# Optimization experiments

Hardware: AMD Instinct MI355X
Metric: run time of the kernel (lower is better)

## Reference

```python
import jax, jax.numpy as jnp
import numpy as np
from jax import lax

B, L, N_NODES, N_SEQ = 256, 15360, 16, 64


def _lstm_layer(x, wih, whh, bih, bhh):
    # x: (B, T, I); torch gate order i, f, g, o
    H = whh.shape[1]
    b = bih + bhh
    def step(carry, xt):
        h, c = carry
        gates = xt @ wih.T + h @ whh.T + b
        i, f, g, o = jnp.split(gates, 4, axis=-1)
        c = jax.nn.sigmoid(f) * c + jax.nn.sigmoid(i) * jnp.tanh(g)
        h = jax.nn.sigmoid(o) * jnp.tanh(c)
        return (h, c), h
    h0 = jnp.zeros((x.shape[0], H), x.dtype)
    _, ys = lax.scan(step, (h0, h0), x.transpose(1, 0, 2))
    return ys.transpose(1, 0, 2)


def setup_inputs() -> dict:
    ks = iter(jax.random.split(jax.random.key(0), 64))
    def rn(shape, scale=1.0):
        return (jax.random.normal(next(ks), shape) * scale).astype(jnp.float32)
    d = {"x": rn((B, 1, L))}
    chs = [1, 16, 32, 64]
    for i in range(3):
        cin, cout = chs[i], chs[i + 1]
        s = 1.0 / np.sqrt(cin * 5)
        d[f"cw{i}"] = rn((cout, cin, 5), s)
        d[f"cb{i}"] = rn((cout,), s)
        d[f"bng{i}"] = jnp.ones((cout,), jnp.float32)
        d[f"bnb{i}"] = jnp.zeros((cout,), jnp.float32)
        d[f"bnm{i}"] = jnp.zeros((cout,), jnp.float32)
        d[f"bnv{i}"] = jnp.ones((cout,), jnp.float32)
    Hh = 64
    for l in range(2):
        s = 1.0 / np.sqrt(Hh)
        d[f"wih{l}"] = rn((4 * Hh, 64), s)
        d[f"whh{l}"] = rn((4 * Hh, Hh), s)
        d[f"bih{l}"] = rn((4 * Hh,), s)
        d[f"bhh{l}"] = rn((4 * Hh,), s)
    gin = [256, 64, 64]
    for l in range(3):
        s = 1.0 / np.sqrt(gin[l])
        d[f"gw{l}"] = rn((64, gin[l]), s)
        d[f"gb{l}"] = rn((64,), s)
    d["clw"] = rn((5, 64), 0.125)
    d["clb"] = rn((5,), 0.125)
    return d


def reference(x, cw0, cb0, bng0, bnb0, bnm0, bnv0, cw1, cb1, bng1, bnb1, bnm1, bnv1, cw2, cb2, bng2, bnb2, bnm2, bnv2, wih0, whh0, bih0, bhh0, wih1, whh1, bih1, bhh1, gw0, gb0, gw1, gb1, gw2, gb2, clw, clb):
    h = x
    # CNN: [Conv1d(k=5,p=2) -> BN(eval) -> ReLU -> MaxPool(2)] x 3
    for cw, cb, g, b, m, v in ((cw0, cb0, bng0, bnb0, bnm0, bnv0),
                               (cw1, cb1, bng1, bnb1, bnm1, bnv1),
                               (cw2, cb2, bng2, bnb2, bnm2, bnv2)):
        h = lax.conv_general_dilated(h, cw, (1,), [(2, 2)], dimension_numbers=("NCH", "OIH", "NCH")) + cb[None, :, None]
        h = g[None, :, None] * (h - m[None, :, None]) * lax.rsqrt(v[None, :, None] + 1e-5) + b[None, :, None]
        h = jax.nn.relu(h)
        Bq, Cq, Lq = h.shape
        h = h.reshape(Bq, Cq, Lq // 2, 2).max(-1)
    # AdaptiveAvgPool1d(64): length divisible by 64 -> exact mean bins
    Bq, Cq, Lq = h.shape
    h = h.reshape(Bq, Cq, N_SEQ, Lq // N_SEQ).mean(-1)
    h = h.transpose(0, 2, 1)  # (B, 64, 64) = (batch, seq, channels)
    # 2-layer LSTM (dropout is identity in eval)
    h = _lstm_layer(h, wih0, whh0, bih0, bhh0)
    h = _lstm_layer(h, wih1, whh1, bih1, bhh1)
    # Graph builder: Pearson-style correlation + value thresholding
    Hf = h.reshape(Bq, -1)
    fpn = Hf.shape[1] // N_NODES  # 256 features per node
    nf = Hf[:, :N_NODES * fpn].reshape(Bq, N_NODES, fpn)
    cen = nf - nf.mean(-1, keepdims=True)
    nrm = cen / (jnp.std(cen, axis=-1, ddof=1, keepdims=True) + 1e-8)
    C = jnp.einsum("bnf,bmf->bnm", nrm, nrm) / fpn  # (B, N, N)
    Cf = C.reshape(Bq, -1)
    k = min(max(1, int((100.0 - 25.0) / 100.0 * Cf.shape[1])), Cf.shape[1] - 1)
    thr = jnp.sort(Cf, axis=1)[:, k - 1]  # torch.kthvalue(k)
    eye = jnp.eye(N_NODES, dtype=C.dtype)
    adj = (C > thr[:, None, None]).astype(C.dtype) * (1.0 - eye)
    # GCN: x = ReLU(W (x + A x) + b), 3 layers, then max over nodes
    g = nf
    for gw, gb in ((gw0, gb0), (gw1, gb1), (gw2, gb2)):
        g = jax.nn.relu((g + jnp.einsum("bnm,bmf->bnf", adj, g)) @ gw.T + gb)
    emb = g.max(axis=1)
    return emb @ clw.T + clb
```

## Files before the change

kernel.cpp:

```cpp
#include <hip/hip_runtime.h>
#include <math.h>

typedef __attribute__((ext_vector_type(2))) float v2f;

__global__ __launch_bounds__(256) void prep_weights_kernel(
    const float* __restrict__ cw0, const float* __restrict__ cb0,
    const float* __restrict__ bng0, const float* __restrict__ bnb0,
    const float* __restrict__ bnm0, const float* __restrict__ bnv0,
    const float* __restrict__ cw1, const float* __restrict__ cb1,
    const float* __restrict__ bng1, const float* __restrict__ bnb1,
    const float* __restrict__ bnm1, const float* __restrict__ bnv1,
    const float* __restrict__ cw2, const float* __restrict__ cb2,
    const float* __restrict__ bng2, const float* __restrict__ bnb2,
    const float* __restrict__ bnm2, const float* __restrict__ bnv2,
    float* __restrict__ wt1, float* __restrict__ b1,
    float* __restrict__ wt2, float* __restrict__ b2,
    float* __restrict__ w0f, float* __restrict__ b0f)
{
    int tid = threadIdx.x;
    for (int i = tid; i < 2560; i += 256) {
        int co = i & 31, r = i >> 5, t = r % 5, ci = r / 5;
        float s = bng1[co] * rsqrtf(bnv1[co] + 1e-5f);
        wt1[i] = cw1[(co * 16 + ci) * 5 + t] * s;
    }
    if (tid < 32) {
        float s = bng1[tid] * rsqrtf(bnv1[tid] + 1e-5f);
        b1[tid] = (cb1[tid] - bnm1[tid]) * s + bnb1[tid];
    }
    for (int i = tid; i < 10240; i += 256) {
        int co = i & 63, r = i >> 6, t = r % 5, ci = r / 5;
        float s = bng2[co] * rsqrtf(bnv2[co] + 1e-5f);
        wt2[i] = cw2[(co * 32 + ci) * 5 + t] * s;
    }
    if (tid < 64) {
        float s = bng2[tid] * rsqrtf(bnv2[tid] + 1e-5f);
        b2[tid] = (cb2[tid] - bnm2[tid]) * s + bnb2[tid];
    }
    if (tid < 80) {
        int co = tid / 5;
        float s = bng0[co] * rsqrtf(bnv0[co] + 1e-5f);
        w0f[tid] = cw0[tid] * s;
    }
    if (tid < 16) {
        float s = bng0[tid] * rsqrtf(bnv0[tid] + 1e-5f);
        b0f[tid] = (cb0[tid] - bnm0[tid]) * s + bnb0[tid];
    }
}

__global__ __launch_bounds__(256) void conv01_kernel(
    const float* __restrict__ x, const float* __restrict__ wt1,
    const float* __restrict__ b1, const float* __restrict__ w0f,
    const float* __restrict__ b0f, float* __restrict__ out)
{
    __shared__ float raw[528];
    __shared__ float xt0[16][260];
    __shared__ float w0l[80];
    __shared__ float b0l[16];
    int b = blockIdx.y, tid = threadIdx.x;
    int j0 = blockIdx.x * 128;
    const float* xb = x + (size_t)b * 15360;
    for (int p = tid; p < 524; p += 256) {
        int g = 4 * j0 - 6 + p;
        raw[p] = (g >= 0 && g < 15360) ? xb[g] : 0.f;
    }
    if (tid < 80) w0l[tid] = w0f[tid];
    if (tid < 16) b0l[tid] = b0f[tid];
    __syncthreads();
    {
        int ci0 = tid >> 4, sub = tid & 15;
        float w0 = w0l[ci0 * 5 + 0], w1 = w0l[ci0 * 5 + 1], w2 = w0l[ci0 * 5 + 2],
              w3 = w0l[ci0 * 5 + 3], w4 = w0l[ci0 * 5 + 4];
        float bb = b0l[ci0];
        for (int p = sub; p < 260; p += 16) {
            int q = 2 * j0 - 2 + p;
            float v = 0.f;
            if (q >= 0 && q < 7680) {
                float r0 = raw[2*p], r1 = raw[2*p+1], r2 = raw[2*p+2],
                      r3 = raw[2*p+3], r4 = raw[2*p+4], r5 = raw[2*p+5];
                float s0 = fmaf(w0, r0, fmaf(w1, r1, fmaf(w2, r2, fmaf(w3, r3, w4 * r4))));
                float s1 = fmaf(w0, r1, fmaf(w1, r2, fmaf(w2, r3, fmaf(w3, r4, w4 * r5))));
                v = fmaxf(fmaxf(s0, s1) + bb, 0.f);
            }
            xt0[ci0][p] = v;
        }
    }
    __syncthreads();
    int cg = tid >> 7, jj = tid & 127;
    int cgu = __builtin_amdgcn_readfirstlane(cg);
    const float* wb = wt1 + cgu * 16;
    v2f a0[8], a1[8];
#pragma unroll
    for (int q = 0; q < 8; ++q) { a0[q] = (v2f){0.f, 0.f}; a1[q] = (v2f){0.f, 0.f}; }
#pragma unroll 4
    for (int ci = 0; ci < 16; ++ci) {
        const float2* xr = reinterpret_cast<const float2*>(&xt0[ci][0]);
        float2 xA = xr[jj], xB = xr[jj + 1], xC = xr[jj + 2];
        float xv[6] = { xA.x, xA.y, xB.x, xB.y, xC.x, xC.y };
#pragma unroll
        for (int t = 0; t < 5; ++t) {
            const v2f* wp2 = reinterpret_cast<const v2f*>(wb + (ci * 5 + t) * 32);
            v2f va = { xv[t], xv[t] };
            v2f vc = { xv[t + 1], xv[t + 1] };
#pragma unroll
            for (int q2 = 0; q2 < 8; ++q2) {
                v2f w = wp2[q2];
                a0[q2] = __builtin_elementwise_fma(w, va, a0[q2]);
                a1[q2] = __builtin_elementwise_fma(w, vc, a1[q2]);
            }
        }
    }
    int j = j0 + jj;
    size_t obase = ((size_t)b * 32 + cgu * 16) * 3840 + j;
#pragma unroll
    for (int q2 = 0; q2 < 8; ++q2) {
#pragma unroll
        for (int cpp = 0; cpp < 2; ++cpp) {
            int q = 2 * q2 + cpp;
            float vb = b1[cgu * 16 + q];
            float m = fmaxf(a0[q2][cpp], a1[q2][cpp]) + vb;
            out[obase + (size_t)q * 3840] = fmaxf(m, 0.f);
        }
    }
}

__global__ __launch_bounds__(256) void conv2p_kernel(
    const float* __restrict__ in, const float* __restrict__ wt2,
    const float* __restrict__ b2, float* __restrict__ xs)
{
    __shared__ float xt[32 * 132];
    int b = blockIdx.y, tid = threadIdx.x;
    int j0 = blockIdx.x * 60;
    {
        int ci = tid >> 3, lane8 = tid & 7;
        const float* src = in + ((size_t)b * 32 + ci) * 3840;
        for (int p = lane8; p < 132; p += 8) {
            int gp = 2 * j0 - 2 + p;
            xt[ci * 132 + p] = (gp >= 0 && gp < 3840) ? src[gp] : 0.f;
        }
    }
    __syncthreads();
    int cg = tid >> 6, jj = tid & 63;
    int cgu = __builtin_amdgcn_readfirstlane(cg);
    const float* wb = wt2 + cgu * 16;
    v2f a0[8], a1[8];
#pragma unroll
    for (int q = 0; q < 8; ++q) { a0[q] = (v2f){0.f, 0.f}; a1[q] = (v2f){0.f, 0.f}; }
#pragma unroll 4
    for (int ci = 0; ci < 32; ++ci) {
        const float2* xr = reinterpret_cast<const float2*>(xt + ci * 132);
        float2 xA = xr[jj], xB = xr[jj + 1], xC = xr[jj + 2];
        float xv[6] = { xA.x, xA.y, xB.x, xB.y, xC.x, xC.y };
#pragma unroll
        for (int t = 0; t < 5; ++t) {
            const v2f* wp2 = reinterpret_cast<const v2f*>(wb + (ci * 5 + t) * 64);
            v2f va = { xv[t], xv[t] };
            v2f vc = { xv[t + 1], xv[t + 1] };
#pragma unroll
            for (int q2 = 0; q2 < 8; ++q2) {
                v2f w = wp2[q2];
                a0[q2] = __builtin_elementwise_fma(w, va, a0[q2]);
                a1[q2] = __builtin_elementwise_fma(w, vc, a1[q2]);
            }
        }
    }
    __syncthreads();
    float* outt = xt;
    if (jj < 60) {
#pragma unroll
        for (int q2 = 0; q2 < 8; ++q2) {
#pragma unroll
            for (int cpp = 0; cpp < 2; ++cpp) {
                int q = 2 * q2 + cpp;
                int co = cgu * 16 + q;
                float m = fmaxf(a0[q2][cpp], a1[q2][cpp]) + b2[co];
                outt[co * 61 + jj] = fmaxf(m, 0.f);
            }
        }
    }
    __syncthreads();
    if (tid < 128) {
        int co = tid & 63, bin = tid >> 6;
        const float* r = outt + co * 61 + bin * 30;
        float s = 0.f;
#pragma unroll
        for (int k = 0; k < 30; ++k) s += r[k];
        xs[((size_t)b * 64 + (blockIdx.x * 2 + bin)) * 64 + co] = s * (1.f / 30.f);
    }
}

__global__ __launch_bounds__(256) void lstm_kernel(
    const float* __restrict__ xseq,
    const float* __restrict__ wih0, const float* __restrict__ whh0,
    const float* __restrict__ bih0, const float* __restrict__ bhh0,
    const float* __restrict__ wih1, const float* __restrict__ whh1,
    const float* __restrict__ bih1, const float* __restrict__ bhh1,
    float* __restrict__ hseq)
{
    __shared__ float xb[64][64];
    __shared__ float xg[64][256];
    __shared__ float gb4[4][64];
    __shared__ float hb[64];
    int b = blockIdx.x;
    int tid = threadIdx.x;
    int wv = tid >> 6, ln = tid & 63;
    for (int i = tid; i < 4096; i += 256) xb[i >> 6][i & 63] = xseq[(size_t)b * 4096 + i];
    __syncthreads();
    float wr[64];
    for (int layer = 0; layer < 2; ++layer) {
        const float* wih = layer ? wih1 : wih0;
        const float* whh = layer ? whh1 : whh0;
        float bias = layer ? (bih1[tid] + bhh1[tid]) : (bih0[tid] + bhh0[tid]);
#pragma unroll
        for (int k4 = 0; k4 < 16; ++k4) {
            float4 v = reinterpret_cast<const float4*>(wih + (size_t)tid * 64)[k4];
            wr[k4 * 4 + 0] = v.x; wr[k4 * 4 + 1] = v.y;
            wr[k4 * 4 + 2] = v.z; wr[k4 * 4 + 3] = v.w;
        }
        for (int t = 0; t < 64; ++t) {
            float s0 = bias, s1 = 0.f, s2 = 0.f, s3 = 0.f;
#pragma unroll
            for (int k = 0; k < 64; k += 4) {
                s0 = fmaf(wr[k + 0], xb[t][k + 0], s0);
                s1 = fmaf(wr[k + 1], xb[t][k + 1], s1);
                s2 = fmaf(wr[k + 2], xb[t][k + 2], s2);
                s3 = fmaf(wr[k + 3], xb[t][k + 3], s3);
            }
            xg[t][tid] = (s0 + s1) + (s2 + s3);
        }
#pragma unroll
        for (int k4 = 0; k4 < 16; ++k4) {
            float4 v = reinterpret_cast<const float4*>(whh + (size_t)tid * 64)[k4];
            wr[k4 * 4 + 0] = v.x; wr[k4 * 4 + 1] = v.y;
            wr[k4 * 4 + 2] = v.z; wr[k4 * 4 + 3] = v.w;
        }
        if (tid < 64) hb[tid] = 0.f;
        float c = 0.f;
        __syncthreads();
        for (int t = 0; t < 64; ++t) {
            float s0 = xg[t][tid], s1 = 0.f, s2 = 0.f, s3 = 0.f;
#pragma unroll
            for (int k = 0; k < 64; k += 4) {
                s0 = fmaf(wr[k + 0], hb[k + 0], s0);
                s1 = fmaf(wr[k + 1], hb[k + 1], s1);
                s2 = fmaf(wr[k + 2], hb[k + 2], s2);
                s3 = fmaf(wr[k + 3], hb[k + 3], s3);
            }
            float acc = (s0 + s1) + (s2 + s3);
            float a;
            if (wv == 2) a = tanhf(acc);
            else         a = 1.f / (1.f + __expf(-acc));
            gb4[wv][ln] = a;
            __syncthreads();
            float gi = gb4[0][ln], gf = gb4[1][ln], gg = gb4[2][ln], go = gb4[3][ln];
            c = fmaf(gf, c, gi * gg);
            float h = go * tanhf(c);
            if (wv == 0) {
                hb[ln] = h;
                if (layer == 0) xb[t][ln] = h;
                else hseq[((size_t)b * 64 + t) * 64 + ln] = h;
            }
            __syncthreads();
        }
    }
}

__global__ __launch_bounds__(256) void graph_kernel(
    const float* __restrict__ hseq,
    const float* __restrict__ gw0, const float* __restrict__ gb0,
    const float* __restrict__ gw1, const float* __restrict__ gb1,
    const float* __restrict__ gw2, const float* __restrict__ gb2,
    const float* __restrict__ clw, const float* __restrict__ clb,
    float* __restrict__ out)
{
    __shared__ float nf[16][257];
    __shared__ float sb[16][257];
    __shared__ float red[16][17];
    __shared__ float mean[16], rstd[16];
    __shared__ float C[256];
    __shared__ float adj[16][16];
    __shared__ float thrv;
    __shared__ float bufA[16][65], bufB[16][65], bufC[16][65];
    __shared__ float emb[64];
    int b = blockIdx.x, tid = threadIdx.x;
    for (int i = tid; i < 4096; i += 256) nf[i >> 8][i & 255] = hseq[(size_t)b * 4096 + i];
    __syncthreads();
    int nd = tid >> 4, sub = tid & 15;
    {
        float s = 0.f;
        for (int f = sub; f < 256; f += 16) s += nf[nd][f];
        red[nd][sub] = s;
    }
    __syncthreads();
    if (tid < 16) {
        float m = 0.f;
        for (int i = 0; i < 16; ++i) m += red[tid][i];
        mean[tid] = m * (1.f / 256.f);
    }
    __syncthreads();
    {
        float mu = mean[nd];
        float ss = 0.f;
        for (int f = sub; f < 256; f += 16) { float d = nf[nd][f] - mu; ss = fmaf(d, d, ss); }
        red[nd][sub] = ss;
    }
    __syncthreads();
    if (tid < 16) {
        float m = 0.f;
        for (int i = 0; i < 16; ++i) m += red[tid][i];
        rstd[tid] = 1.f / (sqrtf(m * (1.f / 255.f)) + 1e-8f);
    }
    __syncthreads();
    for (int i = tid; i < 4096; i += 256) {
        int n = i >> 8, f = i & 255;
        sb[n][f] = (nf[n][f] - mean[n]) * rstd[n];
    }
    __syncthreads();
    {
        int n = tid >> 4, m = tid & 15;
        float a0 = 0, a1 = 0, a2 = 0, a3 = 0;
        for (int f = 0; f < 256; f += 4) {
            a0 = fmaf(sb[n][f + 0], sb[m][f + 0], a0);
            a1 = fmaf(sb[n][f + 1], sb[m][f + 1], a1);
            a2 = fmaf(sb[n][f + 2], sb[m][f + 2], a2);
            a3 = fmaf(sb[n][f + 3], sb[m][f + 3], a3);
        }
        C[tid] = ((a0 + a1) + (a2 + a3)) * (1.f / 256.f);
    }
    __syncthreads();
    {
        float v = C[tid];
        int cnt = 0, eq = 0;
        for (int j2 = 0; j2 < 256; ++j2) {
            float vj = C[j2];
            cnt += (vj < v);
            eq  += (vj == v);
        }
        if (cnt <= 191 && 191 < cnt + eq) thrv = v;
    }
    __syncthreads();
    {
        int n = tid >> 4, m = tid & 15;
        adj[n][m] = (C[tid] > thrv && n != m) ? 1.f : 0.f;
    }
    __syncthreads();
    for (int i = tid; i < 4096; i += 256) {
        int n = i >> 8, f = i & 255;
        float acc = nf[n][f];
#pragma unroll
        for (int m = 0; m < 16; ++m) acc = fmaf(adj[n][m], nf[m][f], acc);
        sb[n][f] = acc;
    }
    __syncthreads();
    for (int i = tid; i < 1024; i += 256) {
        int n = i >> 6, o = i & 63;
        const float4* wr4 = reinterpret_cast<const float4*>(gw0 + (size_t)o * 256);
        float acc = gb0[o];
        for (int f4 = 0; f4 < 64; ++f4) {
            float4 wv = wr4[f4];
            int f = f4 * 4;
            acc = fmaf(sb[n][f + 0], wv.x, acc);
            acc = fmaf(sb[n][f + 1], wv.y, acc);
            acc = fmaf(sb[n][f + 2], wv.z, acc);
            acc = fmaf(sb[n][f + 3], wv.w, acc);
        }
        bufA[n][o] = fmaxf(acc, 0.f);
    }
    __syncthreads();
    for (int i = tid; i < 1024; i += 256) {
        int n = i >> 6, f = i & 63;
        float acc = bufA[n][f];
#pragma unroll
        for (int m = 0; m < 16; ++m) acc = fmaf(adj[n][m], bufA[m][f], acc);
        bufB[n][f] = acc;
    }
    __syncthreads();
    for (int i = tid; i < 1024; i += 256) {
        int n = i >> 6, o = i & 63;
        const float4* wr4 = reinterpret_cast<const float4*>(gw1 + (size_t)o * 64);
        float acc = gb1[o];
        for (int f4 = 0; f4 < 16; ++f4) {
            float4 wv = wr4[f4];
            int f = f4 * 4;
            acc = fmaf(bufB[n][f + 0], wv.x, acc);
            acc = fmaf(bufB[n][f + 1], wv.y, acc);
            acc = fmaf(bufB[n][f + 2], wv.z, acc);
            acc = fmaf(bufB[n][f + 3], wv.w, acc);
        }
        bufC[n][o] = fmaxf(acc, 0.f);
    }
    __syncthreads();
    for (int i = tid; i < 1024; i += 256) {
        int n = i >> 6, f = i & 63;
        float acc = bufC[n][f];
#pragma unroll
        for (int m = 0; m < 16; ++m) acc = fmaf(adj[n][m], bufC[m][f], acc);
        bufA[n][f] = acc;
    }
    __syncthreads();
    for (int i = tid; i < 1024; i += 256) {
        int n = i >> 6, o = i & 63;
        const float4* wr4 = reinterpret_cast<const float4*>(gw2 + (size_t)o * 64);
        float acc = gb2[o];
        for (int f4 = 0; f4 < 16; ++f4) {
            float4 wv = wr4[f4];
            int f = f4 * 4;
            acc = fmaf(bufA[n][f + 0], wv.x, acc);
            acc = fmaf(bufA[n][f + 1], wv.y, acc);
            acc = fmaf(bufA[n][f + 2], wv.z, acc);
            acc = fmaf(bufA[n][f + 3], wv.w, acc);
        }
        bufB[n][o] = fmaxf(acc, 0.f);
    }
    __syncthreads();
    if (tid < 64) {
        float mx = bufB[0][tid];
#pragma unroll
        for (int n = 1; n < 16; ++n) mx = fmaxf(mx, bufB[n][tid]);
        emb[tid] = mx;
    }
    __syncthreads();
    if (tid < 5) {
        float acc = clb[tid];
#pragma unroll
        for (int o = 0; o < 64; ++o) acc = fmaf(emb[o], clw[tid * 64 + o], acc);
        out[(size_t)b * 5 + tid] = acc;
    }
}

extern "C" void kernel_launch(void* const* d_in, const int* in_sizes, int n_in,
                              void* d_out, int out_size, void* d_ws, size_t ws_size,
                              hipStream_t stream)
{
    const float* x    = (const float*)d_in[0];
    const float* cw0  = (const float*)d_in[1];
    const float* cb0  = (const float*)d_in[2];
    const float* bng0 = (const float*)d_in[3];
    const float* bnb0 = (const float*)d_in[4];
    const float* bnm0 = (const float*)d_in[5];
    const float* bnv0 = (const float*)d_in[6];
    const float* cw1  = (const float*)d_in[7];
    const float* cb1  = (const float*)d_in[8];
    const float* bng1 = (const float*)d_in[9];
    const float* bnb1 = (const float*)d_in[10];
    const float* bnm1 = (const float*)d_in[11];
    const float* bnv1 = (const float*)d_in[12];
    const float* cw2  = (const float*)d_in[13];
    const float* cb2  = (const float*)d_in[14];
    const float* bng2 = (const float*)d_in[15];
    const float* bnb2 = (const float*)d_in[16];
    const float* bnm2 = (const float*)d_in[17];
    const float* bnv2 = (const float*)d_in[18];
    const float* wih0 = (const float*)d_in[19];
    const float* whh0 = (const float*)d_in[20];
    const float* bih0 = (const float*)d_in[21];
    const float* bhh0 = (const float*)d_in[22];
    const float* wih1 = (const float*)d_in[23];
    const float* whh1 = (const float*)d_in[24];
    const float* bih1 = (const float*)d_in[25];
    const float* bhh1 = (const float*)d_in[26];
    const float* gw0  = (const float*)d_in[27];
    const float* gb0  = (const float*)d_in[28];
    const float* gw1  = (const float*)d_in[29];
    const float* gb1  = (const float*)d_in[30];
    const float* gw2  = (const float*)d_in[31];
    const float* gb2  = (const float*)d_in[32];
    const float* clw  = (const float*)d_in[33];
    const float* clb  = (const float*)d_in[34];

    float* f0  = (float*)d_ws;
    float* xs  = f0 + 31457280;
    float* hs  = xs + 1048576;
    float* wt1 = hs + 1048576;
    float* b1  = wt1 + 2560;
    float* wt2 = b1 + 32;
    float* b2  = wt2 + 10240;
    float* w0f = b2 + 64;
    float* b0f = w0f + 80;

    prep_weights_kernel<<<1, 256, 0, stream>>>(
        cw0, cb0, bng0, bnb0, bnm0, bnv0,
        cw1, cb1, bng1, bnb1, bnm1, bnv1,
        cw2, cb2, bng2, bnb2, bnm2, bnv2,
        wt1, b1, wt2, b2, w0f, b0f);
    conv01_kernel<<<dim3(30, 256), 256, 0, stream>>>(x, wt1, b1, w0f, b0f, f0);
    conv2p_kernel<<<dim3(32, 256), 256, 0, stream>>>(f0, wt2, b2, xs);
    lstm_kernel<<<256, 256, 0, stream>>>(xs, wih0, whh0, bih0, bhh0,
                                         wih1, whh1, bih1, bhh1, hs);
    graph_kernel<<<256, 256, 0, stream>>>(hs, gw0, gb0, gw1, gb1, gw2, gb2,
                                          clw, clb, (float*)d_out);
}
```

Measured before the change: 483.1 us.

## Fuse all three conv stages into one kernel with halo recompute in LDS

Merges the conv0+conv1 kernel and the conv2+pool kernel into a single kernel that keeps the conv1 output tile in shared memory, recomputing halo columns per block. This removes the round trip of the 32-channel intermediate (about 126 MB) through global memory and one launch. The cost is a slightly larger recompute of overlapping conv0/conv1 columns and more LDS per block. It also vectorizes the LSTM shared-memory reads into float4 loads.

```diff
diff --git a/kernel.cpp b/kernel.cpp
--- a/kernel.cpp
+++ b/kernel.cpp
@@ -47,144 +47,136 @@
     }
 }
 
-__global__ __launch_bounds__(256) void conv01_kernel(
-    const float* __restrict__ x, const float* __restrict__ wt1,
-    const float* __restrict__ b1, const float* __restrict__ w0f,
-    const float* __restrict__ b0f, float* __restrict__ out)
+__global__ __launch_bounds__(256) void convall_kernel(
+    const float* __restrict__ x,
+    const float* __restrict__ w0f, const float* __restrict__ b0f,
+    const float* __restrict__ wt1, const float* __restrict__ b1,
+    const float* __restrict__ wt2, const float* __restrict__ b2,
+    float* __restrict__ xs)
 {
-    __shared__ float raw[528];
-    __shared__ float xt0[16][260];
-    __shared__ float w0l[80];
-    __shared__ float b0l[16];
-    int b = blockIdx.y, tid = threadIdx.x;
-    int j0 = blockIdx.x * 128;
+    __shared__ float raw[512];
+    __shared__ float U[8320];
+    int b = blockIdx.y, bx = blockIdx.x, tid = threadIdx.x;
     const float* xb = x + (size_t)b * 15360;
-    for (int p = tid; p < 524; p += 256) {
-        int g = 4 * j0 - 6 + p;
-        raw[p] = (g >= 0 && g < 15360) ? xb[g] : 0.f;
-    }
-    if (tid < 80) w0l[tid] = w0f[tid];
-    if (tid < 16) b0l[tid] = b0f[tid];
+    {
+        int base = 480 * bx - 14;
+        for (int i = tid; i < 508; i += 256) {
+            int g = base + i;
+            raw[i] = (g >= 0 && g < 15360) ? xb[g] : 0.f;
+        }
+    }
     __syncthreads();
     {
         int ci0 = tid >> 4, sub = tid & 15;
-        float w0 = w0l[ci0 * 5 + 0], w1 = w0l[ci0 * 5 + 1], w2 = w0l[ci0 * 5 + 2],
-              w3 = w0l[ci0 * 5 + 3], w4 = w0l[ci0 * 5 + 4];
-        float bb = b0l[ci0];
-        for (int p = sub; p < 260; p += 16) {
-            int q = 2 * j0 - 2 + p;
+        float w0 = w0f[ci0*5+0], w1 = w0f[ci0*5+1], w2 = w0f[ci0*5+2],
+              w3 = w0f[ci0*5+3], w4 = w0f[ci0*5+4];
+        float bb = b0f[ci0];
+        int r0g = 240 * bx - 6;
+        for (int p = sub; p < 252; p += 16) {
+            int r = r0g + p;
             float v = 0.f;
-            if (q >= 0 && q < 7680) {
-                float r0 = raw[2*p], r1 = raw[2*p+1], r2 = raw[2*p+2],
-                      r3 = raw[2*p+3], r4 = raw[2*p+4], r5 = raw[2*p+5];
-                float s0 = fmaf(w0, r0, fmaf(w1, r1, fmaf(w2, r2, fmaf(w3, r3, w4 * r4))));
-                float s1 = fmaf(w0, r1, fmaf(w1, r2, fmaf(w2, r3, fmaf(w3, r4, w4 * r5))));
+            if (r >= 0 && r < 7680) {
+                int i0 = 2 * p;
+                float c0 = raw[i0],   c1 = raw[i0+1], c2 = raw[i0+2],
+                      c3 = raw[i0+3], c4 = raw[i0+4], c5 = raw[i0+5];
+                float s0 = fmaf(w0,c0, fmaf(w1,c1, fmaf(w2,c2, fmaf(w3,c3, w4*c4))));
+                float s1 = fmaf(w0,c1, fmaf(w1,c2, fmaf(w2,c3, fmaf(w3,c4, w4*c5))));
                 v = fmaxf(fmaxf(s0, s1) + bb, 0.f);
             }
-            xt0[ci0][p] = v;
-        }
-    }
-    __syncthreads();
-    int cg = tid >> 7, jj = tid & 127;
-    int cgu = __builtin_amdgcn_readfirstlane(cg);
-    const float* wb = wt1 + cgu * 16;
-    v2f a0[8], a1[8];
-#pragma unroll
-    for (int q = 0; q < 8; ++q) { a0[q] = (v2f){0.f, 0.f}; a1[q] = (v2f){0.f, 0.f}; }
+            U[ci0 * 256 + p] = v;
+        }
+    }
+    __syncthreads();
+    {
+        int cg = tid >> 7, jj = tid & 127;
+        int cgu = __builtin_amdgcn_readfirstlane(cg);
+        { int co = tid >> 3, c = 124 + (tid & 7); U[4096 + co * 132 + c] = 0.f; }
+        if (jj < 124) {
+            const float* wb = wt1 + cgu * 16;
+            v2f a0[8], a1[8];
+#pragma unroll
+            for (int q = 0; q < 8; ++q) { a0[q] = (v2f){0.f,0.f}; a1[q] = (v2f){0.f,0.f}; }
 #pragma unroll 4
-    for (int ci = 0; ci < 16; ++ci) {
-        const float2* xr = reinterpret_cast<const float2*>(&xt0[ci][0]);
-        float2 xA = xr[jj], xB = xr[jj + 1], xC = xr[jj + 2];
-        float xv[6] = { xA.x, xA.y, xB.x, xB.y, xC.x, xC.y };
-#pragma unroll
-        for (int t = 0; t < 5; ++t) {
-            const v2f* wp2 = reinterpret_cast<const v2f*>(wb + (ci * 5 + t) * 32);
-            v2f va = { xv[t], xv[t] };
-            v2f vc = { xv[t + 1], xv[t + 1] };
+            for (int ci = 0; ci < 16; ++ci) {
+                const float2* xr = reinterpret_cast<const float2*>(&U[ci * 256]);
+                float2 xA = xr[jj], xB = xr[jj + 1], xC = xr[jj + 2];
+                float xv[6] = { xA.x, xA.y, xB.x, xB.y, xC.x, xC.y };
+#pragma unroll
+                for (int t = 0; t < 5; ++t) {
+                    const v2f* wp2 = reinterpret_cast<const v2f*>(wb + (ci * 5 + t) * 32);
+                    v2f va = { xv[t], xv[t] };
+                    v2f vc = { xv[t + 1], xv[t + 1] };
+#pragma unroll
+                    for (int q2 = 0; q2 < 8; ++q2) {
+                        v2f w = wp2[q2];
+                        a0[q2] = __builtin_elementwise_fma(w, va, a0[q2]);
+                        a1[q2] = __builtin_elementwise_fma(w, vc, a1[q2]);
+                    }
+                }
+            }
+            int q = 120 * bx - 2 + jj;
+            bool ok = (q >= 0 && q < 3840);
 #pragma unroll
             for (int q2 = 0; q2 < 8; ++q2) {
-                v2f w = wp2[q2];
-                a0[q2] = __builtin_elementwise_fma(w, va, a0[q2]);
-                a1[q2] = __builtin_elementwise_fma(w, vc, a1[q2]);
-            }
-        }
-    }
-    int j = j0 + jj;
-    size_t obase = ((size_t)b * 32 + cgu * 16) * 3840 + j;
-#pragma unroll
-    for (int q2 = 0; q2 < 8; ++q2) {
-#pragma unroll
-        for (int cpp = 0; cpp < 2; ++cpp) {
-            int q = 2 * q2 + cpp;
-            float vb = b1[cgu * 16 + q];
-            float m = fmaxf(a0[q2][cpp], a1[q2][cpp]) + vb;
-            out[obase + (size_t)q * 3840] = fmaxf(m, 0.f);
-        }
-    }
-}
-
-__global__ __launch_bounds__(256) void conv2p_kernel(
-    const float* __restrict__ in, const float* __restrict__ wt2,
-    const float* __restrict__ b2, float* __restrict__ xs)
-{
-    __shared__ float xt[32 * 132];
-    int b = blockIdx.y, tid = threadIdx.x;
-    int j0 = blockIdx.x * 60;
-    {
-        int ci = tid >> 3, lane8 = tid & 7;
-        const float* src = in + ((size_t)b * 32 + ci) * 3840;
-        for (int p = lane8; p < 132; p += 8) {
-            int gp = 2 * j0 - 2 + p;
-            xt[ci * 132 + p] = (gp >= 0 && gp < 3840) ? src[gp] : 0.f;
-        }
-    }
-    __syncthreads();
-    int cg = tid >> 6, jj = tid & 63;
-    int cgu = __builtin_amdgcn_readfirstlane(cg);
-    const float* wb = wt2 + cgu * 16;
-    v2f a0[8], a1[8];
-#pragma unroll
-    for (int q = 0; q < 8; ++q) { a0[q] = (v2f){0.f, 0.f}; a1[q] = (v2f){0.f, 0.f}; }
+#pragma unroll
+                for (int cpp = 0; cpp < 2; ++cpp) {
+                    int qq = 2 * q2 + cpp;
+                    int co = cgu * 16 + qq;
+                    float val = 0.f;
+                    if (ok) val = fmaxf(fmaxf(a0[q2][cpp], a1[q2][cpp]) + b1[co], 0.f);
+                    U[4096 + co * 132 + jj] = val;
+                }
+            }
+        }
+    }
+    __syncthreads();
+    {
+        int cg = tid >> 6, jj = tid & 63;
+        int cgu = __builtin_amdgcn_readfirstlane(cg);
+        const float* wb = wt2 + cgu * 16;
+        v2f a0[8], a1[8];
+#pragma unroll
+        for (int q = 0; q < 8; ++q) { a0[q] = (v2f){0.f,0.f}; a1[q] = (v2f){0.f,0.f}; }
 #pragma unroll 4
-    for (int ci = 0; ci < 32; ++ci) {
-        const float2* xr = reinterpret_cast<const float2*>(xt + ci * 132);
-        float2 xA = xr[jj], xB = xr[jj + 1], xC = xr[jj + 2];
-        float xv[6] = { xA.x, xA.y, xB.x, xB.y, xC.x, xC.y };
-#pragma unroll
-        for (int t = 0; t < 5; ++t) {
-            const v2f* wp2 = reinterpret_cast<const v2f*>(wb + (ci * 5 + t) * 64);
-            v2f va = { xv[t], xv[t] };
-            v2f vc = { xv[t + 1], xv[t + 1] };
+        for (int ci = 0; ci < 32; ++ci) {
+            const float2* xr = reinterpret_cast<const float2*>(&U[4096 + ci * 132]);
+            float2 xA = xr[jj], xB = xr[jj + 1], xC = xr[jj + 2];
+            float xv[6] = { xA.x, xA.y, xB.x, xB.y, xC.x, xC.y };
+#pragma unroll
+            for (int t = 0; t < 5; ++t) {
+                const v2f* wp2 = reinterpret_cast<const v2f*>(wb + (ci * 5 + t) * 64);
+                v2f va = { xv[t], xv[t] };
+                v2f vc = { xv[t + 1], xv[t + 1] };
+#pragma unroll
+                for (int q2 = 0; q2 < 8; ++q2) {
+                    v2f w = wp2[q2];
+                    a0[q2] = __builtin_elementwise_fma(w, va, a0[q2]);
+                    a1[q2] = __builtin_elementwise_fma(w, vc, a1[q2]);
+                }
+            }
+        }
+        __syncthreads();
+        if (jj < 60) {
 #pragma unroll
             for (int q2 = 0; q2 < 8; ++q2) {
-                v2f w = wp2[q2];
-                a0[q2] = __builtin_elementwise_fma(w, va, a0[q2]);
-                a1[q2] = __builtin_elementwise_fma(w, vc, a1[q2]);
-            }
-        }
-    }
-    __syncthreads();
-    float* outt = xt;
-    if (jj < 60) {
-#pragma unroll
-        for (int q2 = 0; q2 < 8; ++q2) {
-#pragma unroll
-            for (int cpp = 0; cpp < 2; ++cpp) {
-                int q = 2 * q2 + cpp;
-                int co = cgu * 16 + q;
-                float m = fmaxf(a0[q2][cpp], a1[q2][cpp]) + b2[co];
-                outt[co * 61 + jj] = fmaxf(m, 0.f);
+#pragma unroll
+                for (int cpp = 0; cpp < 2; ++cpp) {
+                    int qq = 2 * q2 + cpp;
+                    int co = cgu * 16 + qq;
+                    float m = fmaxf(a0[q2][cpp], a1[q2][cpp]) + b2[co];
+                    U[co * 61 + jj] = fmaxf(m, 0.f);
+                }
             }
         }
     }
     __syncthreads();
     if (tid < 128) {
         int co = tid & 63, bin = tid >> 6;
-        const float* r = outt + co * 61 + bin * 30;
+        const float* r = U + co * 61 + bin * 30;
         float s = 0.f;
 #pragma unroll
         for (int k = 0; k < 30; ++k) s += r[k];
-        xs[((size_t)b * 64 + (blockIdx.x * 2 + bin)) * 64 + co] = s * (1.f / 30.f);
+        xs[((size_t)b * 64 + (bx * 2 + bin)) * 64 + co] = s * (1.f / 30.f);
     }
 }
 
@@ -219,11 +211,12 @@
         for (int t = 0; t < 64; ++t) {
             float s0 = bias, s1 = 0.f, s2 = 0.f, s3 = 0.f;
 #pragma unroll
-            for (int k = 0; k < 64; k += 4) {
-                s0 = fmaf(wr[k + 0], xb[t][k + 0], s0);
-                s1 = fmaf(wr[k + 1], xb[t][k + 1], s1);
-                s2 = fmaf(wr[k + 2], xb[t][k + 2], s2);
-                s3 = fmaf(wr[k + 3], xb[t][k + 3], s3);
+            for (int k4 = 0; k4 < 16; ++k4) {
+                float4 xv4 = *reinterpret_cast<const float4*>(&xb[t][k4 * 4]);
+                s0 = fmaf(wr[k4 * 4 + 0], xv4.x, s0);
+                s1 = fmaf(wr[k4 * 4 + 1], xv4.y, s1);
+                s2 = fmaf(wr[k4 * 4 + 2], xv4.z, s2);
+                s3 = fmaf(wr[k4 * 4 + 3], xv4.w, s3);
             }
             xg[t][tid] = (s0 + s1) + (s2 + s3);
         }
@@ -239,11 +232,12 @@
         for (int t = 0; t < 64; ++t) {
             float s0 = xg[t][tid], s1 = 0.f, s2 = 0.f, s3 = 0.f;
 #pragma unroll
-            for (int k = 0; k < 64; k += 4) {
-                s0 = fmaf(wr[k + 0], hb[k + 0], s0);
-                s1 = fmaf(wr[k + 1], hb[k + 1], s1);
-                s2 = fmaf(wr[k + 2], hb[k + 2], s2);
-                s3 = fmaf(wr[k + 3], hb[k + 3], s3);
+            for (int k4 = 0; k4 < 16; ++k4) {
+                float4 hv4 = *reinterpret_cast<const float4*>(&hb[k4 * 4]);
+                s0 = fmaf(wr[k4 * 4 + 0], hv4.x, s0);
+                s1 = fmaf(wr[k4 * 4 + 1], hv4.y, s1);
+                s2 = fmaf(wr[k4 * 4 + 2], hv4.z, s2);
+                s3 = fmaf(wr[k4 * 4 + 3], hv4.w, s3);
             }
             float acc = (s0 + s1) + (s2 + s3);
             float a;
@@ -467,8 +461,7 @@
     const float* clw  = (const float*)d_in[33];
     const float* clb  = (const float*)d_in[34];
 
-    float* f0  = (float*)d_ws;
-    float* xs  = f0 + 31457280;
+    float* xs  = (float*)d_ws;
     float* hs  = xs + 1048576;
     float* wt1 = hs + 1048576;
     float* b1  = wt1 + 2560;
@@ -482,8 +475,7 @@
         cw1, cb1, bng1, bnb1, bnm1, bnv1,
         cw2, cb2, bng2, bnb2, bnm2, bnv2,
         wt1, b1, wt2, b2, w0f, b0f);
-    conv01_kernel<<<dim3(30, 256), 256, 0, stream>>>(x, wt1, b1, w0f, b0f, f0);
-    conv2p_kernel<<<dim3(32, 256), 256, 0, stream>>>(f0, wt2, b2, xs);
+    convall_kernel<<<dim3(32, 256), 256, 0, stream>>>(x, w0f, b0f, wt1, b1, wt2, b2, xs);
     lstm_kernel<<<256, 256, 0, stream>>>(xs, wih0, whh0, bih0, bhh0,
                                          wih1, whh1, bih1, bhh1, hs);
     graph_kernel<<<256, 256, 0, stream>>>(hs, gw0, gb0, gw1, gb1, gw2, gb2,
```

New measurement: 478.0 us. No clear change (-1.1%).
